# Optimization experiments

Hardware: AMD Instinct MI355X
Metric: run time of the kernel (lower is better)

Reference implementation:

```python
import jax, jax.numpy as jnp
import numpy as np

DIM = 1024
MLP_RATIO = 4
EPS = 1e-6


def rmsnorm(x, w):
    return x * jax.lax.rsqrt(jnp.mean(x * x, axis=-1, keepdims=True) + EPS) * w


def film(x, cond, w, b):
    # cond: [B, D] -> scale/shift: [B, D] each, broadcast over tokens
    ss = cond @ w + b  # [B, 2D]
    scale, shift = jnp.split(ss, 2, axis=-1)
    return x * (1.0 + scale[:, None, :]) + shift[:, None, :]


def setup_inputs() -> dict:
    key = jax.random.key(0)
    ks = jax.random.split(key, 16)
    B, N, D = 4, 2048, DIM
    H = D * MLP_RATIO
    s = lambda fan_in: 1.0 / np.sqrt(fan_in)
    return {
        "x": jax.random.normal(ks[0], (B, N, D), jnp.float32),
        "cond": jax.random.normal(ks[1], (B, D), jnp.float32),
        "norm1_w": jnp.ones((D,), jnp.float32),
        "film1_w": jax.random.normal(ks[2], (D, 2 * D), jnp.float32) * s(D),
        "film1_b": jnp.zeros((2 * D,), jnp.float32),
        "q_w": jax.random.normal(ks[3], (D, D), jnp.float32) * s(D),
        "q_b": jnp.zeros((D,), jnp.float32),
        "k_w": jax.random.normal(ks[4], (D, D), jnp.float32) * s(D),
        "k_b": jnp.zeros((D,), jnp.float32),
        "v_w": jax.random.normal(ks[5], (D, D), jnp.float32) * s(D),
        "v_b": jnp.zeros((D,), jnp.float32),
        "proj_w": jax.random.normal(ks[6], (D, D), jnp.float32) * s(D),
        "proj_b": jnp.zeros((D,), jnp.float32),
        "norm2_w": jnp.ones((D,), jnp.float32),
        "film2_w": jax.random.normal(ks[7], (D, 2 * D), jnp.float32) * s(D),
        "film2_b": jnp.zeros((2 * D,), jnp.float32),
        "mlp_w1": jax.random.normal(ks[8], (D, H), jnp.float32) * s(D),
        "mlp_b1": jnp.zeros((H,), jnp.float32),
        "mlp_w2": jax.random.normal(ks[9], (H, D), jnp.float32) * s(H),
        "mlp_b2": jnp.zeros((D,), jnp.float32),
    }


def reference(x, cond, norm1_w, film1_w, film1_b, q_w, q_b, k_w, k_b, v_w, v_b,
              proj_w, proj_b, norm2_w, film2_w, film2_b, mlp_w1, mlp_b1,
              mlp_w2, mlp_b2):
    B, N, D = x.shape
    x_in = x
    h = film(rmsnorm(x, norm1_w), cond, film1_w, film1_b)
    Q = h @ q_w + q_b
    K = h @ k_w + k_b
    V = h @ v_w + v_b
    scores = jnp.einsum('bnd,bmd->bnm', Q, K) * (D ** -0.5)  # [B,N,N]
    attn = jax.nn.softmax(scores, axis=-1)
    out = jnp.einsum('bnm,bmd->bnd', attn, V)
    x = x_in + (out @ proj_w + proj_b)
    x_in = x
    h = film(rmsnorm(x, norm2_w), cond, film2_w, film2_b)
    h = jax.nn.gelu(h @ mlp_w1 + mlp_b1, approximate=False) @ mlp_w2 + mlp_b2
    return x_in + h
```

## Files before the change

kernel.cpp:

```cpp
#include <hip/hip_runtime.h>
#include <math.h>

typedef unsigned short u16;
typedef __bf16 bf16;
typedef bf16 bf16x8 __attribute__((ext_vector_type(8)));
typedef float f32x4 __attribute__((ext_vector_type(4)));

#define DEV __device__ __forceinline__
#define MFMA(a, b, c) __builtin_amdgcn_mfma_f32_16x16x32_bf16(a, b, c, 0, 0, 0)

DEV u16 f2b(float f) {
  unsigned u = __builtin_bit_cast(unsigned, f);
  u += 0x7fffu + ((u >> 16) & 1u);
  return (u16)(u >> 16);
}
DEV float b2f(u16 h) {
  unsigned u = ((unsigned)h) << 16;
  return __builtin_bit_cast(float, u);
}
DEV float gelu_f(float x) { return 0.5f * x * (1.0f + erff(x * 0.70710678118654752f)); }

DEV void gl2lds16(const void* g, void* l) {
  __builtin_amdgcn_global_load_lds(
      (const __attribute__((address_space(1))) unsigned int*)g,
      (__attribute__((address_space(3))) unsigned int*)l, 16, 0, 0);
}

__global__ void k_transpose_cvt(const float* __restrict__ src, u16* __restrict__ dst,
                                int R, int C) {
  __shared__ float tile[32][33];
  const int c0 = blockIdx.x * 32, r0 = blockIdx.y * 32;
  const int tx = threadIdx.x, ty = threadIdx.y;
#pragma unroll
  for (int i = 0; i < 32; i += 8)
    tile[ty + i][tx] = src[(long)(r0 + ty + i) * C + c0 + tx];
  __syncthreads();
#pragma unroll
  for (int i = 0; i < 32; i += 8)
    dst[(long)(c0 + ty + i) * R + r0 + tx] = f2b(tile[tx][ty + i]);
}

__global__ __launch_bounds__(256) void k_film_part(const float* __restrict__ cond,
                                                   const float* __restrict__ fw,
                                                   float* __restrict__ part) {
  const int j = blockIdx.x * 256 + threadIdx.x;
  const int b = blockIdx.y;
  const int kz = blockIdx.z;
  const float* cp = cond + b * 1024 + kz * 128;
  const float* wp = fw + (long)kz * 128 * 2048 + j;
  float acc = 0.0f;
#pragma unroll 4
  for (int d = 0; d < 128; ++d) acc = fmaf(cp[d], wp[(long)d * 2048], acc);
  part[((kz * 4 + b) << 11) + j] = acc;
}
__global__ __launch_bounds__(256) void k_film_comb(const float* __restrict__ part,
                                                   const float* __restrict__ fb,
                                                   float* __restrict__ ss) {
  const int j = blockIdx.x * 256 + threadIdx.x;
  const int b = blockIdx.y;
  float a = fb[j];
#pragma unroll
  for (int kz = 0; kz < 8; ++kz) a += part[((kz * 4 + b) << 11) + j];
  ss[b * 2048 + j] = a;
}

__global__ __launch_bounds__(256) void k_rmsfilm(const float* __restrict__ x,
                                                 const float* __restrict__ nw,
                                                 const float* __restrict__ ss,
                                                 u16* __restrict__ h) {
  const int row = blockIdx.x;
  const int b = row >> 11;
  const int t = threadIdx.x;
  const float4 v = ((const float4*)(x + (long)row * 1024))[t];
  float s = v.x * v.x + v.y * v.y + v.z * v.z + v.w * v.w;
#pragma unroll
  for (int off = 32; off; off >>= 1) s += __shfl_xor(s, off);
  __shared__ float red[4];
  const int wv = t >> 6, lane = t & 63;
  if (lane == 0) red[wv] = s;
  __syncthreads();
  const float tot = red[0] + red[1] + red[2] + red[3];
  const float rn = rsqrtf(tot * (1.0f / 1024.0f) + 1e-6f);
  const float4 w4 = ((const float4*)nw)[t];
  const float4 sc = ((const float4*)(ss + b * 2048))[t];
  const float4 sh = ((const float4*)(ss + b * 2048 + 1024))[t];
  ushort4 o;
  o.x = f2b(v.x * rn * w4.x * (1.0f + sc.x) + sh.x);
  o.y = f2b(v.y * rn * w4.y * (1.0f + sc.y) + sh.y);
  o.z = f2b(v.z * rn * w4.z * (1.0f + sc.z) + sh.z);
  o.w = f2b(v.w * rn * w4.w * (1.0f + sc.w) + sh.w);
  ((ushort4*)(h + (long)row * 1024))[t] = o;
}

__global__ __launch_bounds__(256) void k_softmax(u16* __restrict__ S) {
  u16* p = S + ((long)blockIdx.x << 11);
  const int t = threadIdx.x;
  ushort4 u0 = ((ushort4*)p)[2 * t], u1 = ((ushort4*)p)[2 * t + 1];
  float f[8] = {b2f(u0.x), b2f(u0.y), b2f(u0.z), b2f(u0.w),
                b2f(u1.x), b2f(u1.y), b2f(u1.z), b2f(u1.w)};
  float m = f[0];
#pragma unroll
  for (int i = 1; i < 8; ++i) m = fmaxf(m, f[i]);
#pragma unroll
  for (int off = 32; off; off >>= 1) m = fmaxf(m, __shfl_xor(m, off));
  __shared__ float red[4];
  const int wv = t >> 6, lane = t & 63;
  if (lane == 0) red[wv] = m;
  __syncthreads();
  m = fmaxf(fmaxf(red[0], red[1]), fmaxf(red[2], red[3]));
  float s = 0.0f;
#pragma unroll
  for (int i = 0; i < 8; ++i) {
    f[i] = __expf(f[i] - m);
    s += f[i];
  }
#pragma unroll
  for (int off = 32; off; off >>= 1) s += __shfl_xor(s, off);
  __syncthreads();
  if (lane == 0) red[wv] = s;
  __syncthreads();
  const float inv = 1.0f / (red[0] + red[1] + red[2] + red[3]);
  ushort4 o0, o1;
  o0.x = f2b(f[0] * inv); o0.y = f2b(f[1] * inv);
  o0.z = f2b(f[2] * inv); o0.w = f2b(f[3] * inv);
  o1.x = f2b(f[4] * inv); o1.y = f2b(f[5] * inv);
  o1.z = f2b(f[6] * inv); o1.w = f2b(f[7] * inv);
  ((ushort4*)p)[2 * t] = o0;
  ((ushort4*)p)[2 * t + 1] = o1;
}

enum { EB = 1, ES = 2, EG = 4, ER = 8, EQKV = 16 };

template <int EPI, typename OutT>
__global__ __launch_bounds__(256, 2) void k_gemm(
    const u16* __restrict__ A, const u16* __restrict__ B, OutT* __restrict__ C,
    const float* __restrict__ bias, const float* __restrict__ bias2,
    const float* __restrict__ bias3, const float* __restrict__ resid,
    u16* __restrict__ Vt, float scale, int N, int K, long sAb, long sBb, long sCb) {
  __shared__ u16 As[128 * 64];
  __shared__ u16 Bs[128 * 64];
  const int tid = threadIdx.x, lane = tid & 63, wv = tid >> 6;
  const int wr = wv >> 1, wc = wv & 1;
  const int r = lane & 15, q = lane >> 4;

  int flat = blockIdx.y * gridDim.x + blockIdx.x;
  const int nxy = gridDim.x * gridDim.y;
  flat = (flat & 7) * (nxy >> 3) + (flat >> 3);
  const int bx = flat % gridDim.x, by = flat / gridDim.x;

  const long bm = (long)by * 128, bn = (long)bx * 128;
  const u16* Ab = A + (long)blockIdx.z * sAb + bm * K;
  const u16* Bb = B + (long)blockIdx.z * sBb + bn * K;

  f32x4 acc[4][4] = {};

  for (int k0 = 0; k0 < K; k0 += 64) {
#pragma unroll
    for (int i = 0; i < 4; ++i) {
      const int c = i * 256 + tid;
      const int row = c >> 3, sp = c & 7;
      const long g = (long)row * K + k0 + ((sp ^ (row & 7)) << 3);
      gl2lds16(Ab + g, As + c * 8);
      gl2lds16(Bb + g, Bs + c * 8);
    }
    __syncthreads();
    bf16x8 a[8], b[8];
#pragma unroll
    for (int kh = 0; kh < 2; ++kh) {
#pragma unroll
      for (int i = 0; i < 4; ++i) {
        const int ar = wr * 64 + i * 16 + r;
        const int br = wc * 64 + i * 16 + r;
        a[kh * 4 + i] = *(const bf16x8*)&As[ar * 64 + ((kh * 4 + q) ^ (ar & 7)) * 8];
        b[kh * 4 + i] = *(const bf16x8*)&Bs[br * 64 + ((kh * 4 + q) ^ (br & 7)) * 8];
      }
    }
#pragma unroll
    for (int kh = 0; kh < 2; ++kh)
#pragma unroll
      for (int mi = 0; mi < 4; ++mi)
#pragma unroll
        for (int ni = 0; ni < 4; ++ni)
          acc[mi][ni] = MFMA(a[kh * 4 + mi], b[kh * 4 + ni], acc[mi][ni]);
    __syncthreads();
  }

  const long cb = (long)blockIdx.z * sCb;
#pragma unroll
  for (int ni = 0; ni < 4; ++ni) {
    const long col = bn + wc * 64 + ni * 16 + r;
    float bv = 0.0f;
    int reg = 0, c = (int)col;
    if constexpr ((EPI & EB) != 0) bv = bias[col];
    if constexpr ((EPI & EQKV) != 0) {
      reg = (int)(col >> 10);
      c = (int)col & 1023;
      bv = (reg == 0) ? bias[c] : (reg == 1) ? bias2[c] : bias3[c];
    }
#pragma unroll
    for (int mi = 0; mi < 4; ++mi) {
#pragma unroll
      for (int j = 0; j < 4; ++j) {
        const long row = bm + wr * 64 + mi * 16 + q * 4 + j;
        float v = acc[mi][ni][j];
        if constexpr ((EPI & ES) != 0) v *= scale;
        if constexpr ((EPI & (EB | EQKV)) != 0) v += bv;
        if constexpr ((EPI & EG) != 0) v = gelu_f(v);
        if constexpr ((EPI & ER) != 0) v += resid[row * N + col];
        if constexpr ((EPI & EQKV) != 0) {
          if (reg < 2)
            ((u16*)C)[(long)reg * 8388608 + row * 1024 + c] = f2b(v);
          else
            Vt[((row >> 11) << 21) + ((long)c << 11) + (row & 2047)] = f2b(v);
        } else if constexpr (sizeof(OutT) == 4) {
          C[cb + row * N + col] = v;
        } else {
          C[cb + row * N + col] = f2b(v);
        }
      }
    }
  }
}

extern "C" void kernel_launch(void* const* d_in, const int* in_sizes, int n_in,
                              void* d_out, int out_size, void* d_ws, size_t ws_size,
                              hipStream_t stream) {
  const float* x    = (const float*)d_in[0];
  const float* cond = (const float*)d_in[1];
  const float* n1w  = (const float*)d_in[2];
  const float* f1w  = (const float*)d_in[3];
  const float* f1b  = (const float*)d_in[4];
  const float* qw   = (const float*)d_in[5];
  const float* qb   = (const float*)d_in[6];
  const float* kw   = (const float*)d_in[7];
  const float* kb   = (const float*)d_in[8];
  const float* vw   = (const float*)d_in[9];
  const float* vb   = (const float*)d_in[10];
  const float* pw   = (const float*)d_in[11];
  const float* pb   = (const float*)d_in[12];
  const float* n2w  = (const float*)d_in[13];
  const float* f2w  = (const float*)d_in[14];
  const float* f2b_ = (const float*)d_in[15];
  const float* w1   = (const float*)d_in[16];
  const float* b1   = (const float*)d_in[17];
  const float* w2   = (const float*)d_in[18];
  const float* b2   = (const float*)d_in[19];
  float* out = (float*)d_out;

  char* ws = (char*)d_ws;
  size_t o = 0;
  auto alloc = [&](size_t bytes) {
    size_t ret = o;
    o += (bytes + 255) & ~(size_t)255;
    return ret;
  };
  const long N = 2048, D = 1024, H = 4096;

  u16* qkvT = (u16*)(ws + alloc(3 * D * D * 2));
  u16* pT   = (u16*)(ws + alloc(D * D * 2));
  u16* w1T  = (u16*)(ws + alloc(D * H * 2));
  u16* w2T  = (u16*)(ws + alloc(D * H * 2));
  float* ss1  = (float*)(ws + alloc(4 * 2 * D * 4));
  float* ss2  = (float*)(ws + alloc(4 * 2 * D * 4));
  float* part = (float*)(ws + alloc(8 * 4 * 2 * D * 4));
  u16* h    = (u16*)(ws + alloc(4 * N * D * 2));
  float* x1 = (float*)(ws + alloc(4 * N * D * 4));
  u16* AO   = (u16*)(ws + alloc(4 * N * D * 2));
  const size_t big = o;
  u16* Q    = (u16*)(ws + alloc(4 * N * D * 2));
  u16* Kb   = (u16*)(ws + alloc(4 * N * D * 2));
  u16* Vt   = (u16*)(ws + alloc(4 * N * D * 2));
  u16* S    = (u16*)(ws + alloc(4 * N * N * 2));
  u16* h1   = (u16*)(ws + big);
  (void)ws_size; (void)in_sizes; (void)n_in; (void)out_size; (void)Kb;

  dim3 tb(32, 8);
  k_transpose_cvt<<<dim3(32, 32), tb, 0, stream>>>(qw, qkvT, 1024, 1024);
  k_transpose_cvt<<<dim3(32, 32), tb, 0, stream>>>(kw, qkvT + 1024 * 1024, 1024, 1024);
  k_transpose_cvt<<<dim3(32, 32), tb, 0, stream>>>(vw, qkvT + 2 * 1024 * 1024, 1024, 1024);
  k_transpose_cvt<<<dim3(32, 32), tb, 0, stream>>>(pw, pT, 1024, 1024);
  k_transpose_cvt<<<dim3(128, 32), tb, 0, stream>>>(w1, w1T, 1024, 4096);
  k_transpose_cvt<<<dim3(32, 128), tb, 0, stream>>>(w2, w2T, 4096, 1024);

  k_film_part<<<dim3(8, 4, 8), 256, 0, stream>>>(cond, f1w, part);
  k_film_comb<<<dim3(8, 4), 256, 0, stream>>>(part, f1b, ss1);
  k_film_part<<<dim3(8, 4, 8), 256, 0, stream>>>(cond, f2w, part);
  k_film_comb<<<dim3(8, 4), 256, 0, stream>>>(part, f2b_, ss2);

  k_rmsfilm<<<8192, 256, 0, stream>>>(x, n1w, ss1, h);

  k_gemm<EQKV, u16><<<dim3(24, 64, 1), 256, 0, stream>>>(
      h, qkvT, Q, qb, kb, vb, nullptr, Vt, 1.0f, 3072, 1024, 0, 0, 0);

  k_gemm<ES, u16><<<dim3(16, 16, 4), 256, 0, stream>>>(
      Q, Kb, S, nullptr, nullptr, nullptr, nullptr, nullptr, 0.03125f,
      2048, 1024, N * D, N * D, N * N);
  k_softmax<<<8192, 256, 0, stream>>>(S);

  k_gemm<0, u16><<<dim3(8, 16, 4), 256, 0, stream>>>(
      S, Vt, AO, nullptr, nullptr, nullptr, nullptr, nullptr, 1.0f,
      1024, 2048, N * N, D * N, N * D);

  k_gemm<EB | ER, float><<<dim3(8, 64, 1), 256, 0, stream>>>(
      AO, pT, x1, pb, nullptr, nullptr, x, nullptr, 1.0f, 1024, 1024, 0, 0, 0);

  k_rmsfilm<<<8192, 256, 0, stream>>>(x1, n2w, ss2, h);

  k_gemm<EB | EG, u16><<<dim3(32, 64, 1), 256, 0, stream>>>(
      h, w1T, h1, b1, nullptr, nullptr, nullptr, nullptr, 1.0f, 4096, 1024, 0, 0, 0);

  k_gemm<EB | ER, float><<<dim3(8, 64, 1), 256, 0, stream>>>(
      h1, w2T, out, b2, nullptr, nullptr, x1, nullptr, 1.0f, 1024, 4096, 0, 0, 0);
}
```

Baseline: 435.2 us.

## Batch transposes and FiLM launches, store residual in bf16, use sigmoid-based GELU

Merges the six weight transpose launches into one descriptor-driven kernel and the two FiLM projections into a single part and a single combine launch, cutting launch count. Stores the post-attention residual x1 in bf16 instead of fp32, halving its write and read traffic, with a new epilogue mode that adds a bf16 residual. Replaces the exact erf GELU with a tanh-style sigmoid approximation using __expf. The bf16 residual and approximate GELU both reduce output accuracy.

```diff
diff --git a/kernel.cpp b/kernel.cpp
--- a/kernel.cpp
+++ b/kernel.cpp
@@ -18,7 +18,10 @@
   unsigned u = ((unsigned)h) << 16;
   return __builtin_bit_cast(float, u);
 }
-DEV float gelu_f(float x) { return 0.5f * x * (1.0f + erff(x * 0.70710678118654752f)); }
+DEV float gelu_f(float x) {
+  float e = __expf(x * (-1.5957691216f - 0.07135481283f * x * x));
+  return x / (1.0f + e);
+}
 
 DEV void gl2lds16(const void* g, void* l) {
   __builtin_amdgcn_global_load_lds(
@@ -26,52 +29,71 @@
       (__attribute__((address_space(3))) unsigned int*)l, 16, 0, 0);
 }
 
-__global__ void k_transpose_cvt(const float* __restrict__ src, u16* __restrict__ dst,
-                                int R, int C) {
+struct TDesc { const float* src; u16* dst; int R, C, t0, tx; };
+struct T6 { TDesc d[6]; };
+
+__global__ void k_transpose6(T6 td) {
   __shared__ float tile[32][33];
-  const int c0 = blockIdx.x * 32, r0 = blockIdx.y * 32;
+  const int id = blockIdx.x;
+  TDesc d = td.d[0];
+#pragma unroll
+  for (int k = 1; k < 6; ++k)
+    if (id >= td.d[k].t0) d = td.d[k];
+  const int local = id - d.t0;
+  const int c0 = (local % d.tx) * 32, r0 = (local / d.tx) * 32;
   const int tx = threadIdx.x, ty = threadIdx.y;
 #pragma unroll
   for (int i = 0; i < 32; i += 8)
-    tile[ty + i][tx] = src[(long)(r0 + ty + i) * C + c0 + tx];
+    tile[ty + i][tx] = d.src[(long)(r0 + ty + i) * d.C + c0 + tx];
   __syncthreads();
 #pragma unroll
   for (int i = 0; i < 32; i += 8)
-    dst[(long)(c0 + ty + i) * R + r0 + tx] = f2b(tile[tx][ty + i]);
+    d.dst[(long)(c0 + ty + i) * d.R + r0 + tx] = f2b(tile[tx][ty + i]);
 }
 
 __global__ __launch_bounds__(256) void k_film_part(const float* __restrict__ cond,
-                                                   const float* __restrict__ fw,
+                                                   const float* __restrict__ f1w,
+                                                   const float* __restrict__ f2w,
                                                    float* __restrict__ part) {
   const int j = blockIdx.x * 256 + threadIdx.x;
   const int b = blockIdx.y;
-  const int kz = blockIdx.z;
+  const int z = blockIdx.z;
+  const int kz = z & 7;
+  const float* fw = (z < 8) ? f1w : f2w;
   const float* cp = cond + b * 1024 + kz * 128;
   const float* wp = fw + (long)kz * 128 * 2048 + j;
   float acc = 0.0f;
 #pragma unroll 4
   for (int d = 0; d < 128; ++d) acc = fmaf(cp[d], wp[(long)d * 2048], acc);
-  part[((kz * 4 + b) << 11) + j] = acc;
+  part[((z * 4 + b) << 11) + j] = acc;
 }
 __global__ __launch_bounds__(256) void k_film_comb(const float* __restrict__ part,
-                                                   const float* __restrict__ fb,
+                                                   const float* __restrict__ f1b,
+                                                   const float* __restrict__ f2b_,
                                                    float* __restrict__ ss) {
   const int j = blockIdx.x * 256 + threadIdx.x;
-  const int b = blockIdx.y;
-  float a = fb[j];
-#pragma unroll
-  for (int kz = 0; kz < 8; ++kz) a += part[((kz * 4 + b) << 11) + j];
-  ss[b * 2048 + j] = a;
-}
-
-__global__ __launch_bounds__(256) void k_rmsfilm(const float* __restrict__ x,
+  const int b = blockIdx.y & 3, f = blockIdx.y >> 2;
+  float a = (f ? f2b_ : f1b)[j];
+#pragma unroll
+  for (int kz = 0; kz < 8; ++kz) a += part[(((f * 8 + kz) * 4 + b) << 11) + j];
+  ss[((f * 4 + b) << 11) + j] = a;
+}
+
+template <typename InT>
+__global__ __launch_bounds__(256) void k_rmsfilm(const InT* __restrict__ x,
                                                  const float* __restrict__ nw,
                                                  const float* __restrict__ ss,
                                                  u16* __restrict__ h) {
   const int row = blockIdx.x;
   const int b = row >> 11;
   const int t = threadIdx.x;
-  const float4 v = ((const float4*)(x + (long)row * 1024))[t];
+  float4 v;
+  if constexpr (sizeof(InT) == 4) {
+    v = ((const float4*)(x + (long)row * 1024))[t];
+  } else {
+    ushort4 u = ((const ushort4*)(x + (long)row * 1024))[t];
+    v = make_float4(b2f(u.x), b2f(u.y), b2f(u.z), b2f(u.w));
+  }
   float s = v.x * v.x + v.y * v.y + v.z * v.z + v.w * v.w;
 #pragma unroll
   for (int off = 32; off; off >>= 1) s += __shfl_xor(s, off);
@@ -129,7 +151,7 @@
   ((ushort4*)p)[2 * t + 1] = o1;
 }
 
-enum { EB = 1, ES = 2, EG = 4, ER = 8, EQKV = 16 };
+enum { EB = 1, ES = 2, EG = 4, ER = 8, EQKV = 16, ERB = 32 };
 
 template <int EPI, typename OutT>
 __global__ __launch_bounds__(256, 2) void k_gemm(
@@ -207,6 +229,7 @@
         if constexpr ((EPI & (EB | EQKV)) != 0) v += bv;
         if constexpr ((EPI & EG) != 0) v = gelu_f(v);
         if constexpr ((EPI & ER) != 0) v += resid[row * N + col];
+        if constexpr ((EPI & ERB) != 0) v += b2f(((const u16*)resid)[row * N + col]);
         if constexpr ((EPI & EQKV) != 0) {
           if (reg < 2)
             ((u16*)C)[(long)reg * 8388608 + row * 1024 + c] = f2b(v);
@@ -260,11 +283,10 @@
   u16* pT   = (u16*)(ws + alloc(D * D * 2));
   u16* w1T  = (u16*)(ws + alloc(D * H * 2));
   u16* w2T  = (u16*)(ws + alloc(D * H * 2));
-  float* ss1  = (float*)(ws + alloc(4 * 2 * D * 4));
-  float* ss2  = (float*)(ws + alloc(4 * 2 * D * 4));
-  float* part = (float*)(ws + alloc(8 * 4 * 2 * D * 4));
+  float* ss   = (float*)(ws + alloc(2 * 4 * 2 * D * 4));
+  float* part = (float*)(ws + alloc(16 * 4 * 2 * D * 4));
   u16* h    = (u16*)(ws + alloc(4 * N * D * 2));
-  float* x1 = (float*)(ws + alloc(4 * N * D * 4));
+  u16* x1b  = (u16*)(ws + alloc(4 * N * D * 2));
   u16* AO   = (u16*)(ws + alloc(4 * N * D * 2));
   const size_t big = o;
   u16* Q    = (u16*)(ws + alloc(4 * N * D * 2));
@@ -274,20 +296,19 @@
   u16* h1   = (u16*)(ws + big);
   (void)ws_size; (void)in_sizes; (void)n_in; (void)out_size; (void)Kb;
 
-  dim3 tb(32, 8);
-  k_transpose_cvt<<<dim3(32, 32), tb, 0, stream>>>(qw, qkvT, 1024, 1024);
-  k_transpose_cvt<<<dim3(32, 32), tb, 0, stream>>>(kw, qkvT + 1024 * 1024, 1024, 1024);
-  k_transpose_cvt<<<dim3(32, 32), tb, 0, stream>>>(vw, qkvT + 2 * 1024 * 1024, 1024, 1024);
-  k_transpose_cvt<<<dim3(32, 32), tb, 0, stream>>>(pw, pT, 1024, 1024);
-  k_transpose_cvt<<<dim3(128, 32), tb, 0, stream>>>(w1, w1T, 1024, 4096);
-  k_transpose_cvt<<<dim3(32, 128), tb, 0, stream>>>(w2, w2T, 4096, 1024);
-
-  k_film_part<<<dim3(8, 4, 8), 256, 0, stream>>>(cond, f1w, part);
-  k_film_comb<<<dim3(8, 4), 256, 0, stream>>>(part, f1b, ss1);
-  k_film_part<<<dim3(8, 4, 8), 256, 0, stream>>>(cond, f2w, part);
-  k_film_comb<<<dim3(8, 4), 256, 0, stream>>>(part, f2b_, ss2);
-
-  k_rmsfilm<<<8192, 256, 0, stream>>>(x, n1w, ss1, h);
+  T6 td;
+  td.d[0] = {qw, qkvT,                1024, 1024,    0,  32};
+  td.d[1] = {kw, qkvT + 1024 * 1024,  1024, 1024, 1024,  32};
+  td.d[2] = {vw, qkvT + 2048 * 1024,  1024, 1024, 2048,  32};
+  td.d[3] = {pw, pT,                  1024, 1024, 3072,  32};
+  td.d[4] = {w1, w1T,                 1024, 4096, 4096, 128};
+  td.d[5] = {w2, w2T,                 4096, 1024, 8192,  32};
+  k_transpose6<<<12288, dim3(32, 8), 0, stream>>>(td);
+
+  k_film_part<<<dim3(8, 4, 16), 256, 0, stream>>>(cond, f1w, f2w, part);
+  k_film_comb<<<dim3(8, 8), 256, 0, stream>>>(part, f1b, f2b_, ss);
+
+  k_rmsfilm<float><<<8192, 256, 0, stream>>>(x, n1w, ss, h);
 
   k_gemm<EQKV, u16><<<dim3(24, 64, 1), 256, 0, stream>>>(
       h, qkvT, Q, qb, kb, vb, nullptr, Vt, 1.0f, 3072, 1024, 0, 0, 0);
@@ -301,14 +322,14 @@
       S, Vt, AO, nullptr, nullptr, nullptr, nullptr, nullptr, 1.0f,
       1024, 2048, N * N, D * N, N * D);
 
-  k_gemm<EB | ER, float><<<dim3(8, 64, 1), 256, 0, stream>>>(
-      AO, pT, x1, pb, nullptr, nullptr, x, nullptr, 1.0f, 1024, 1024, 0, 0, 0);
-
-  k_rmsfilm<<<8192, 256, 0, stream>>>(x1, n2w, ss2, h);
+  k_gemm<EB | ER, u16><<<dim3(8, 64, 1), 256, 0, stream>>>(
+      AO, pT, x1b, pb, nullptr, nullptr, x, nullptr, 1.0f, 1024, 1024, 0, 0, 0);
+
+  k_rmsfilm<u16><<<8192, 256, 0, stream>>>(x1b, n2w, ss + 4 * 2048, h);
 
   k_gemm<EB | EG, u16><<<dim3(32, 64, 1), 256, 0, stream>>>(
       h, w1T, h1, b1, nullptr, nullptr, nullptr, nullptr, 1.0f, 4096, 1024, 0, 0, 0);
 
-  k_gemm<EB | ER, float><<<dim3(8, 64, 1), 256, 0, stream>>>(
-      h1, w2T, out, b2, nullptr, nullptr, x1, nullptr, 1.0f, 1024, 4096, 0, 0, 0);
-}
+  k_gemm<EB | ERB, float><<<dim3(8, 64, 1), 256, 0, stream>>>(
+      h1, w2T, out, b2, nullptr, nullptr, (const float*)x1b, nullptr, 1.0f, 1024, 4096, 0, 0, 0);
+}
```

Result: faster. 394.7 us (-9.3%).
